# Performance work log

Hardware: AMD Instinct MI355X
Metric: run time of the kernel (lower is better)

Reference implementation:

```python
import jax, jax.numpy as jnp
import numpy as np

T, N, E = 5, 100000, 1600000
D = 64          # input_dim == lstm hidden_size
H = 64          # hidden_dim (gcn output dim)
FE = 16         # edge_feat_dim


def setup_inputs() -> dict:
    key = jax.random.key(0)
    ks = jax.random.split(key, 12)
    s = 0.05
    return {
        "xs": jax.random.normal(ks[0], (T, N, D), dtype=jnp.float32),
        "edge_index": jax.random.randint(ks[1], (2, E), 0, N, dtype=jnp.int64),
        "edge_attr": jax.random.normal(ks[2], (E, FE), dtype=jnp.float32),
        "init_w": jax.random.normal(ks[3], (D, H), dtype=jnp.float32) * s,
        "w_ih": jax.random.normal(ks[4], (4 * D, D), dtype=jnp.float32) * s,
        "w_hh": jax.random.normal(ks[5], (4 * D, D), dtype=jnp.float32) * s,
        "b_ih": jnp.zeros((4 * D,), dtype=jnp.float32),
        "b_hh": jnp.zeros((4 * D,), dtype=jnp.float32),
        "mlp_w1": jax.random.normal(ks[6], (2 * H + FE, H), dtype=jnp.float32) * s,
        "mlp_b1": jnp.zeros((H,), dtype=jnp.float32),
        "mlp_w2": jax.random.normal(ks[7], (H, 1), dtype=jnp.float32) * s,
        "mlp_b2": jnp.zeros((1,), dtype=jnp.float32),
    }


def reference(xs, edge_index, edge_attr, init_w, w_ih, w_hh, b_ih, b_hh,
              mlp_w1, mlp_b1, mlp_w2, mlp_b2):
    n = xs.shape[1]
    # add_self_loops: append (i,i) for every node
    loops = jnp.arange(n, dtype=edge_index.dtype)
    row = jnp.concatenate([edge_index[0], loops])   # source
    col = jnp.concatenate([edge_index[1], loops])   # target (aggregation index)
    # symmetric GCN normalization based on in-degree over col
    deg = jax.ops.segment_sum(jnp.ones_like(col, dtype=xs.dtype), col, num_segments=n)
    dinv = jnp.where(deg > 0, jax.lax.rsqrt(jnp.maximum(deg, 1.0)) * jnp.where(deg > 0, 1.0, 0.0), 0.0)
    dinv = jnp.where(deg > 0, deg ** -0.5, 0.0)
    norm = dinv[row] * dinv[col]                    # [E+N]

    hd = init_w.shape[1]        # lstm batch = hidden_dim rows of W^T
    hs = w_hh.shape[1]          # lstm hidden size = input_dim
    h0 = jnp.zeros((hd, hs), dtype=xs.dtype)
    c0 = jnp.zeros((hd, hs), dtype=xs.dtype)

    def lstm_step(w, h, c):
        xb = w.T                                    # [hidden_dim, input_dim]
        gates = xb @ w_ih.T + b_ih + h @ w_hh.T + b_hh
        i, f, g, o = jnp.split(gates, 4, axis=-1)   # PyTorch gate order i,f,g,o
        i, f, o = jax.nn.sigmoid(i), jax.nn.sigmoid(f), jax.nn.sigmoid(o)
        g = jnp.tanh(g)
        c = f * c + i * g
        h = o * jnp.tanh(c)
        return h.T, h, c                            # new weight = out.squeeze(1).t()

    def step(carry, x_t):
        w, h, c = carry
        w, h, c = lstm_step(w, h, c)
        xw = x_t @ w                                # [N, H]
        msg = norm[:, None] * xw[row]               # gather + normalize
        agg = jax.ops.segment_sum(msg, col, num_segments=n)  # scatter-add
        x_out = jax.nn.relu(agg)                    # dropout: eval mode -> identity
        return (w, h, c), x_out

    _, xs_out = jax.lax.scan(step, (init_w, h0, c0), xs)
    x_last = xs_out[-1]                             # embeddings of the last graph

    h_src = x_last[edge_index[0]]
    h_dst = x_last[edge_index[1]]
    edge_in = jnp.concatenate([h_src, h_dst, edge_attr], axis=1)  # [E, 2H+FE]
    hid = jax.nn.relu(edge_in @ mlp_w1 + mlp_b1)
    logits = (hid @ mlp_w2 + mlp_b2)[:, 0]
    return logits
```

## Files before the change

kernel.cpp:

```cpp
#include <hip/hip_runtime.h>
#include <hip/hip_bf16.h>
#include <math.h>

#define N_NODES 100000
#define N_EDGES 1600000

#define KP 168
#define KU 160

typedef __attribute__((ext_vector_type(8))) short bf16x8;
typedef __attribute__((ext_vector_type(4))) float f32x4;

__device__ __forceinline__ float sigmoidf_(float x) { return 1.0f / (1.0f + expf(-x)); }
__device__ __forceinline__ unsigned short f2b(float x) {
    __hip_bfloat16 b = __float2bfloat16(x);
    return *(unsigned short*)&b;
}
__device__ __forceinline__ float b2f(unsigned short u) {
    __hip_bfloat16 b = *(__hip_bfloat16*)&u;
    return __bfloat162float(b);
}

__global__ __launch_bounds__(256) void lstm_kernel(
    const float* __restrict__ init_w, const float* __restrict__ w_ih,
    const float* __restrict__ w_hh, const float* __restrict__ b_ih,
    const float* __restrict__ b_hh, float* __restrict__ h_out)
{
    __shared__ float wsum[256 * 65];
    __shared__ float hst[64];
    __shared__ float cst[64];
    __shared__ float gts[256];
    const int t = threadIdx.x;
    const int r = blockIdx.x;

    for (int i = t; i < 256 * 64; i += 256) {
        int g = i >> 6, k = i & 63;
        wsum[g * 65 + k] = w_ih[i] + w_hh[i];
    }
    if (t < 64) hst[t] = init_w[t * 64 + r];
    __syncthreads();

    {
        float acc = b_ih[t] + b_hh[t];
        for (int k = 0; k < 64; ++k) acc += hst[k] * w_ih[t * 64 + k];
        gts[t] = acc;
    }
    __syncthreads();
    if (t < 64) {
        float ig = sigmoidf_(gts[t]);
        float gg = tanhf(gts[128 + t]);
        float og = sigmoidf_(gts[192 + t]);
        float c = ig * gg;
        float h = og * tanhf(c);
        cst[t] = c; hst[t] = h;
    }
    __syncthreads();

    for (int step = 1; step < 5; ++step) {
        float acc = b_ih[t] + b_hh[t];
        for (int k = 0; k < 64; ++k) acc += hst[k] * wsum[t * 65 + k];
        gts[t] = acc;
        __syncthreads();
        if (t < 64) {
            float ig = sigmoidf_(gts[t]);
            float fg = sigmoidf_(gts[64 + t]);
            float gg = tanhf(gts[128 + t]);
            float og = sigmoidf_(gts[192 + t]);
            float c = fg * cst[t] + ig * gg;
            float h = og * tanhf(c);
            cst[t] = c; hst[t] = h;
        }
        __syncthreads();
    }
    if (t < 64) h_out[r * 64 + t] = hst[t];
}

__global__ void deg_kernel(const int* __restrict__ col, int* __restrict__ cnt, int nE)
{
    int i = blockIdx.x * blockDim.x + threadIdx.x;
    int stride = gridDim.x * blockDim.x;
    for (; i < nE; i += stride) atomicAdd(&cnt[col[i]], 1);
}

__global__ void dinv_kernel(const int* __restrict__ cnt, float* __restrict__ dinv, int n)
{
    int i = blockIdx.x * blockDim.x + threadIdx.x;
    int stride = gridDim.x * blockDim.x;
    for (; i < n; i += stride) dinv[i] = rsqrtf((float)(cnt[i] + 1));
}

__global__ __launch_bounds__(1024) void scan_kernel(
    const int* __restrict__ cnt, int* __restrict__ offs, int n)
{
    __shared__ int wsums[16];
    __shared__ int carry_s;
    const int tid = threadIdx.x, lane = tid & 63, wid = tid >> 6;
    if (tid == 0) carry_s = 0;
    __syncthreads();
    for (int base = 0; base < n; base += 4096) {
        int i0 = base + tid * 4;
        int v0 = 0, v1 = 0, v2 = 0, v3 = 0;
        if (i0 + 3 < n) { int4 v = *(const int4*)(cnt + i0); v0 = v.x; v1 = v.y; v2 = v.z; v3 = v.w; }
        else {
            if (i0 < n)     v0 = cnt[i0];
            if (i0 + 1 < n) v1 = cnt[i0 + 1];
            if (i0 + 2 < n) v2 = cnt[i0 + 2];
            if (i0 + 3 < n) v3 = cnt[i0 + 3];
        }
        int tot = v0 + v1 + v2 + v3;
        int s = tot;
        #pragma unroll
        for (int d = 1; d < 64; d <<= 1) { int u = __shfl_up(s, d, 64); if (lane >= d) s += u; }
        if (lane == 63) wsums[wid] = s;
        __syncthreads();
        if (tid == 0) {
            int run = carry_s;
            #pragma unroll
            for (int w = 0; w < 16; ++w) { int u = wsums[w]; wsums[w] = run; run += u; }
            carry_s = run;
        }
        __syncthreads();
        int ex = s - tot + wsums[wid];
        if (i0 < n)     offs[i0]     = ex;
        if (i0 + 1 < n) offs[i0 + 1] = ex + v0;
        if (i0 + 2 < n) offs[i0 + 2] = ex + v0 + v1;
        if (i0 + 3 < n) offs[i0 + 3] = ex + v0 + v1 + v2;
        __syncthreads();
    }
}

__global__ void fill_kernel(const int* __restrict__ row, const int* __restrict__ col,
                            const int* __restrict__ offs, int* __restrict__ fill,
                            int* __restrict__ csr, int nE)
{
    int i = blockIdx.x * blockDim.x + threadIdx.x;
    int stride = gridDim.x * blockDim.x;
    for (; i < nE; i += stride) {
        int c = col[i];
        int pos = atomicAdd(&fill[c], 1);
        csr[offs[c] + pos] = row[i];
    }
}

__global__ __launch_bounds__(256) void xw_kernel(
    const float* __restrict__ x4, const float* __restrict__ h5,
    const float* __restrict__ dinv, unsigned short* __restrict__ y, int n)
{
    __shared__ float wlds[64 * 64];
    const int t = threadIdx.x;
    for (int i = t; i < 4096; i += 256) {
        int j = i >> 6, k = i & 63;
        wlds[k * 64 + j] = h5[i];
    }
    __syncthreads();
    const int lane = t & 63;
    int wv = blockIdx.x * 4 + (t >> 6);
    const int nw = gridDim.x * 4;
    for (int nd = wv; nd < n; nd += nw) {
        float xv = x4[(size_t)nd * 64 + lane];
        float acc = 0.f;
        #pragma unroll
        for (int k = 0; k < 64; ++k) {
            float xk = __shfl(xv, k, 64);
            acc += xk * wlds[k * 64 + lane];
        }
        y[(size_t)nd * 64 + lane] = f2b(acc * dinv[nd]);
    }
}

__global__ __launch_bounds__(256) void gather_kernel(
    const int* __restrict__ offs, const int* __restrict__ cnt,
    const int* __restrict__ csr, const unsigned short* __restrict__ y,
    const float* __restrict__ dinv, unsigned short* __restrict__ xl, int n)
{
    const int lane = threadIdx.x & 63;
    int wv = blockIdx.x * 4 + (threadIdx.x >> 6);
    const int nw = gridDim.x * 4;
    for (int c = wv; c < n; c += nw) {
        float acc = b2f(y[(size_t)c * 64 + lane]);
        int beg = offs[c], num = cnt[c];
        int p = 0;
        for (; p + 4 <= num; p += 4) {
            int r0 = csr[beg + p],     r1 = csr[beg + p + 1];
            int r2 = csr[beg + p + 2], r3 = csr[beg + p + 3];
            float a0 = b2f(y[(size_t)r0 * 64 + lane]);
            float a1 = b2f(y[(size_t)r1 * 64 + lane]);
            float a2 = b2f(y[(size_t)r2 * 64 + lane]);
            float a3 = b2f(y[(size_t)r3 * 64 + lane]);
            acc += (a0 + a1) + (a2 + a3);
        }
        for (; p < num; ++p) acc += b2f(y[(size_t)csr[beg + p] * 64 + lane]);
        xl[(size_t)c * 64 + lane] = f2b(fmaxf(acc * dinv[c], 0.0f));
    }
}

__global__ __launch_bounds__(256) void prep_kernel(const float* __restrict__ w1,
                                                   unsigned short* __restrict__ w1t)
{
    int i = blockIdx.x * 256 + threadIdx.x;
    if (i < 64 * KP) {
        int n = i / KP, k = i - n * KP;
        float v = (k < 144) ? w1[k * 64 + n] : 0.f;
        w1t[i] = f2b(v);
    }
}

__global__ __launch_bounds__(256) void mlp_kernel(
    const unsigned short* __restrict__ xl, const int* __restrict__ ei,
    const float* __restrict__ ea, const unsigned short* __restrict__ w1t,
    const float* __restrict__ b1, const float* __restrict__ w2,
    const float* __restrict__ b2, float* __restrict__ out)
{
    __shared__ unsigned short As[64 * KP];
    __shared__ unsigned short Bs[64 * KP];
    const int t = threadIdx.x;
    const int base = blockIdx.x * 64;

    {
        const uint4* s = (const uint4*)w1t;
        uint4* d = (uint4*)Bs;
        #pragma unroll
        for (int it = 0; it < 6; ++it) {
            int i = t + it * 256;
            if (i < (64 * KP) / 8) d[i] = s[i];
        }
    }
    #pragma unroll
    for (int it = 0; it < 4; ++it) {
        int i = t + it * 256;
        int e = i >> 4, c = i & 15;
        int src = ei[base + e];
        *(uint2*)&As[e * KP + c * 4] = *(const uint2*)&xl[(size_t)src * 64 + c * 4];
    }
    #pragma unroll
    for (int it = 0; it < 4; ++it) {
        int i = t + it * 256;
        int e = i >> 4, c = i & 15;
        int dst = ei[N_EDGES + base + e];
        *(uint2*)&As[e * KP + 64 + c * 4] = *(const uint2*)&xl[(size_t)dst * 64 + c * 4];
    }
    {
        int e = t >> 2, c = t & 3;
        float4 v = *(const float4*)&ea[(size_t)(base + e) * 16 + c * 4];
        ushort4 b;
        b.x = f2b(v.x); b.y = f2b(v.y); b.z = f2b(v.z); b.w = f2b(v.w);
        *(ushort4*)&As[e * KP + 128 + c * 4] = b;
        uint2 z; z.x = 0; z.y = 0;
        *(uint2*)&As[e * KP + 144 + c * 4] = z;
    }
    __syncthreads();

    const int lane = t & 63, w = t >> 6;
    const int col0 = lane & 15, rgrp = lane >> 4;
    const int arow = w * 16 + col0;

    f32x4 acc[4];
    #pragma unroll
    for (int nt = 0; nt < 4; ++nt) acc[nt] = (f32x4){0.f, 0.f, 0.f, 0.f};

    #pragma unroll
    for (int ks = 0; ks < KU / 32; ++ks) {
        int klane = ks * 32 + rgrp * 8;
        bf16x8 a = *(const bf16x8*)&As[arow * KP + klane];
        #pragma unroll
        for (int nt = 0; nt < 4; ++nt) {
            bf16x8 bfr = *(const bf16x8*)&Bs[(nt * 16 + col0) * KP + klane];
            acc[nt] = __builtin_amdgcn_mfma_f32_16x16x32_bf16(a, bfr, acc[nt], 0, 0, 0);
        }
    }

    float bsum = b2[0];
    float part[4];
    #pragma unroll
    for (int j = 0; j < 4; ++j) {
        float s = 0.f;
        #pragma unroll
        for (int nt = 0; nt < 4; ++nt) {
            int nn = nt * 16 + col0;
            s += fmaxf(acc[nt][j] + b1[nn], 0.f) * w2[nn];
        }
        #pragma unroll
        for (int m = 1; m < 16; m <<= 1) s += __shfl_xor(s, m, 64);
        part[j] = s;
    }
    if (col0 == 0) {
        int row = rgrp * 4;
        #pragma unroll
        for (int j = 0; j < 4; ++j)
            out[base + w * 16 + row + j] = part[j] + bsum;
    }
}

extern "C" void kernel_launch(void* const* d_in, const int* in_sizes, int n_in,
                              void* d_out, int out_size, void* d_ws, size_t ws_size,
                              hipStream_t stream)
{
    const float* xs     = (const float*)d_in[0];
    const int*   ei     = (const int*)  d_in[1];
    const float* ea     = (const float*)d_in[2];
    const float* init_w = (const float*)d_in[3];
    const float* w_ih   = (const float*)d_in[4];
    const float* w_hh   = (const float*)d_in[5];
    const float* b_ih   = (const float*)d_in[6];
    const float* b_hh   = (const float*)d_in[7];
    const float* w1     = (const float*)d_in[8];
    const float* b1     = (const float*)d_in[9];
    const float* w2     = (const float*)d_in[10];
    const float* b2     = (const float*)d_in[11];
    float* out = (float*)d_out;

    char* ws = (char*)d_ws;
    size_t off = 0;
    auto alloc = [&](size_t bytes) {
        void* p = ws + off;
        off = (off + bytes + 255) & ~(size_t)255;
        return p;
    };
    float*          h5   = (float*)alloc(64 * 64 * sizeof(float));
    int*            deg  = (int*)  alloc((size_t)N_NODES * sizeof(int));
    int*            fill = (int*)  alloc((size_t)N_NODES * sizeof(int));
    float*          dinv = (float*)alloc((size_t)N_NODES * sizeof(float));
    int*            offs = (int*)  alloc((size_t)N_NODES * sizeof(int));
    int*            csr  = (int*)  alloc((size_t)N_EDGES * sizeof(int));
    unsigned short* y    = (unsigned short*)alloc((size_t)N_NODES * 64 * sizeof(unsigned short));
    unsigned short* xl   = (unsigned short*)alloc((size_t)N_NODES * 64 * sizeof(unsigned short));
    unsigned short* w1t  = (unsigned short*)alloc((size_t)64 * KP * sizeof(unsigned short));

    hipMemsetAsync(deg, 0, (size_t)N_NODES * sizeof(int), stream);
    hipMemsetAsync(fill, 0, (size_t)N_NODES * sizeof(int), stream);

    lstm_kernel<<<64, 256, 0, stream>>>(init_w, w_ih, w_hh, b_ih, b_hh, h5);
    prep_kernel<<<(64 * KP + 255) / 256, 256, 0, stream>>>(w1, w1t);
    deg_kernel<<<1024, 256, 0, stream>>>(ei + N_EDGES, deg, N_EDGES);
    dinv_kernel<<<512, 256, 0, stream>>>(deg, dinv, N_NODES);
    scan_kernel<<<1, 1024, 0, stream>>>(deg, offs, N_NODES);
    fill_kernel<<<1024, 256, 0, stream>>>(ei, ei + N_EDGES, offs, fill, csr, N_EDGES);

    const float* x4 = xs + (size_t)4 * N_NODES * 64;
    xw_kernel<<<2048, 256, 0, stream>>>(x4, h5, dinv, y, N_NODES);
    gather_kernel<<<2048, 256, 0, stream>>>(offs, deg, csr, y, dinv, xl, N_NODES);
    mlp_kernel<<<N_EDGES / 64, 256, 0, stream>>>(xl, ei, ea, w1t, b1, w2, b2, out);
}
```

Baseline: 692.4 us.

## Parallelize CSR scan, vectorize atomics, split gather lanes, register-resident MLP weights

Replaces the single-block degree scan with a three-kernel parallel scan that also writes dinv and initializes fill pointers, which removes the dinv kernel and a memset. Degree and fill kernels now read indices as int4 and use fill as an absolute position. The gather kernel splits each wave into four sub-groups that each process a different neighbor, using 8-byte vector loads, and combines them with cross-lane shuffles. The MLP kernel keeps W1 fragments in registers, loads A fragments straight from global memory with no LDS staging, and uses a persistent grid looping over 16-edge tiles. This raises register pressure and drops LDS reuse of the node embeddings.

```diff
diff --git a/kernel.cpp b/kernel.cpp
--- a/kernel.cpp
+++ b/kernel.cpp
@@ -4,9 +4,7 @@
 
 #define N_NODES 100000
 #define N_EDGES 1600000
-
-#define KP 168
-#define KU 160
+#define NCHUNK 98
 
 typedef __attribute__((ext_vector_type(8))) short bf16x8;
 typedef __attribute__((ext_vector_type(4))) float f32x4;
@@ -75,70 +73,102 @@
     if (t < 64) h_out[r * 64 + t] = hst[t];
 }
 
-__global__ void deg_kernel(const int* __restrict__ col, int* __restrict__ cnt, int nE)
+__global__ void deg_kernel(const int* __restrict__ col, int* __restrict__ cnt, int nE4)
 {
     int i = blockIdx.x * blockDim.x + threadIdx.x;
     int stride = gridDim.x * blockDim.x;
-    for (; i < nE; i += stride) atomicAdd(&cnt[col[i]], 1);
-}
-
-__global__ void dinv_kernel(const int* __restrict__ cnt, float* __restrict__ dinv, int n)
+    for (; i < nE4; i += stride) {
+        int4 c = ((const int4*)col)[i];
+        atomicAdd(&cnt[c.x], 1);
+        atomicAdd(&cnt[c.y], 1);
+        atomicAdd(&cnt[c.z], 1);
+        atomicAdd(&cnt[c.w], 1);
+    }
+}
+
+__global__ __launch_bounds__(256) void scanA_kernel(
+    const int* __restrict__ deg, int* __restrict__ partial,
+    float* __restrict__ dinv, int n)
+{
+    __shared__ int wsums[4];
+    const int t = threadIdx.x, lane = t & 63, wid = t >> 6;
+    int i0 = blockIdx.x * 1024 + t * 4;
+    int v0 = 0, v1 = 0, v2 = 0, v3 = 0;
+    if (i0 + 3 < n) { int4 v = *(const int4*)(deg + i0); v0 = v.x; v1 = v.y; v2 = v.z; v3 = v.w; }
+    else {
+        if (i0 < n)     v0 = deg[i0];
+        if (i0 + 1 < n) v1 = deg[i0 + 1];
+        if (i0 + 2 < n) v2 = deg[i0 + 2];
+        if (i0 + 3 < n) v3 = deg[i0 + 3];
+    }
+    if (i0 < n)     dinv[i0]     = rsqrtf((float)(v0 + 1));
+    if (i0 + 1 < n) dinv[i0 + 1] = rsqrtf((float)(v1 + 1));
+    if (i0 + 2 < n) dinv[i0 + 2] = rsqrtf((float)(v2 + 1));
+    if (i0 + 3 < n) dinv[i0 + 3] = rsqrtf((float)(v3 + 1));
+    int s = v0 + v1 + v2 + v3;
+    #pragma unroll
+    for (int m = 1; m < 64; m <<= 1) s += __shfl_xor(s, m, 64);
+    if (lane == 0) wsums[wid] = s;
+    __syncthreads();
+    if (t == 0) partial[blockIdx.x] = wsums[0] + wsums[1] + wsums[2] + wsums[3];
+}
+
+__global__ void scanB_kernel(int* __restrict__ partial, int nb)
+{
+    __shared__ int w0;
+    const int t = threadIdx.x, lane = t & 63, wid = t >> 6;
+    int v = (t < nb) ? partial[t] : 0;
+    int s = v;
+    #pragma unroll
+    for (int d = 1; d < 64; d <<= 1) { int u = __shfl_up(s, d, 64); if (lane >= d) s += u; }
+    if (t == 63) w0 = s;
+    __syncthreads();
+    int ex = s - v + ((wid == 1) ? w0 : 0);
+    if (t < nb) partial[t] = ex;
+}
+
+__global__ __launch_bounds__(256) void scanC_kernel(
+    const int* __restrict__ deg, const int* __restrict__ partial,
+    int* __restrict__ offs, int* __restrict__ fill, int n)
+{
+    __shared__ int wsums[4];
+    const int t = threadIdx.x, lane = t & 63, wid = t >> 6;
+    int i0 = blockIdx.x * 1024 + t * 4;
+    int v0 = 0, v1 = 0, v2 = 0, v3 = 0;
+    if (i0 + 3 < n) { int4 v = *(const int4*)(deg + i0); v0 = v.x; v1 = v.y; v2 = v.z; v3 = v.w; }
+    else {
+        if (i0 < n)     v0 = deg[i0];
+        if (i0 + 1 < n) v1 = deg[i0 + 1];
+        if (i0 + 2 < n) v2 = deg[i0 + 2];
+        if (i0 + 3 < n) v3 = deg[i0 + 3];
+    }
+    int tot = v0 + v1 + v2 + v3;
+    int s = tot;
+    #pragma unroll
+    for (int d = 1; d < 64; d <<= 1) { int u = __shfl_up(s, d, 64); if (lane >= d) s += u; }
+    if (lane == 63) wsums[wid] = s;
+    __syncthreads();
+    if (t == 0) { int run = 0; for (int w = 0; w < 4; ++w) { int u = wsums[w]; wsums[w] = run; run += u; } }
+    __syncthreads();
+    int ex = s - tot + wsums[wid] + partial[blockIdx.x];
+    if (i0 < n)     { offs[i0]     = ex;                fill[i0]     = ex; }
+    if (i0 + 1 < n) { offs[i0 + 1] = ex + v0;           fill[i0 + 1] = ex + v0; }
+    if (i0 + 2 < n) { offs[i0 + 2] = ex + v0 + v1;      fill[i0 + 2] = ex + v0 + v1; }
+    if (i0 + 3 < n) { offs[i0 + 3] = ex + v0 + v1 + v2; fill[i0 + 3] = ex + v0 + v1 + v2; }
+}
+
+__global__ void fill_kernel(const int* __restrict__ row, const int* __restrict__ col,
+                            int* __restrict__ fill, int* __restrict__ csr, int nE4)
 {
     int i = blockIdx.x * blockDim.x + threadIdx.x;
     int stride = gridDim.x * blockDim.x;
-    for (; i < n; i += stride) dinv[i] = rsqrtf((float)(cnt[i] + 1));
-}
-
-__global__ __launch_bounds__(1024) void scan_kernel(
-    const int* __restrict__ cnt, int* __restrict__ offs, int n)
-{
-    __shared__ int wsums[16];
-    __shared__ int carry_s;
-    const int tid = threadIdx.x, lane = tid & 63, wid = tid >> 6;
-    if (tid == 0) carry_s = 0;
-    __syncthreads();
-    for (int base = 0; base < n; base += 4096) {
-        int i0 = base + tid * 4;
-        int v0 = 0, v1 = 0, v2 = 0, v3 = 0;
-        if (i0 + 3 < n) { int4 v = *(const int4*)(cnt + i0); v0 = v.x; v1 = v.y; v2 = v.z; v3 = v.w; }
-        else {
-            if (i0 < n)     v0 = cnt[i0];
-            if (i0 + 1 < n) v1 = cnt[i0 + 1];
-            if (i0 + 2 < n) v2 = cnt[i0 + 2];
-            if (i0 + 3 < n) v3 = cnt[i0 + 3];
-        }
-        int tot = v0 + v1 + v2 + v3;
-        int s = tot;
-        #pragma unroll
-        for (int d = 1; d < 64; d <<= 1) { int u = __shfl_up(s, d, 64); if (lane >= d) s += u; }
-        if (lane == 63) wsums[wid] = s;
-        __syncthreads();
-        if (tid == 0) {
-            int run = carry_s;
-            #pragma unroll
-            for (int w = 0; w < 16; ++w) { int u = wsums[w]; wsums[w] = run; run += u; }
-            carry_s = run;
-        }
-        __syncthreads();
-        int ex = s - tot + wsums[wid];
-        if (i0 < n)     offs[i0]     = ex;
-        if (i0 + 1 < n) offs[i0 + 1] = ex + v0;
-        if (i0 + 2 < n) offs[i0 + 2] = ex + v0 + v1;
-        if (i0 + 3 < n) offs[i0 + 3] = ex + v0 + v1 + v2;
-        __syncthreads();
-    }
-}
-
-__global__ void fill_kernel(const int* __restrict__ row, const int* __restrict__ col,
-                            const int* __restrict__ offs, int* __restrict__ fill,
-                            int* __restrict__ csr, int nE)
-{
-    int i = blockIdx.x * blockDim.x + threadIdx.x;
-    int stride = gridDim.x * blockDim.x;
-    for (; i < nE; i += stride) {
-        int c = col[i];
-        int pos = atomicAdd(&fill[c], 1);
-        csr[offs[c] + pos] = row[i];
+    for (; i < nE4; i += stride) {
+        int4 c = ((const int4*)col)[i];
+        int4 r = ((const int4*)row)[i];
+        csr[atomicAdd(&fill[c.x], 1)] = r.x;
+        csr[atomicAdd(&fill[c.y], 1)] = r.y;
+        csr[atomicAdd(&fill[c.z], 1)] = r.z;
+        csr[atomicAdd(&fill[c.w], 1)] = r.w;
     }
 }
 
@@ -174,23 +204,45 @@
     const float* __restrict__ dinv, unsigned short* __restrict__ xl, int n)
 {
     const int lane = threadIdx.x & 63;
-    int wv = blockIdx.x * 4 + (threadIdx.x >> 6);
-    const int nw = gridDim.x * 4;
+    const int sub = lane >> 4, q = lane & 15;
+    int wv = (blockIdx.x * 256 + threadIdx.x) >> 6;
+    const int nw = (gridDim.x * 256) >> 6;
     for (int c = wv; c < n; c += nw) {
-        float acc = b2f(y[(size_t)c * 64 + lane]);
-        int beg = offs[c], num = cnt[c];
-        int p = 0;
-        for (; p + 4 <= num; p += 4) {
-            int r0 = csr[beg + p],     r1 = csr[beg + p + 1];
-            int r2 = csr[beg + p + 2], r3 = csr[beg + p + 3];
-            float a0 = b2f(y[(size_t)r0 * 64 + lane]);
-            float a1 = b2f(y[(size_t)r1 * 64 + lane]);
-            float a2 = b2f(y[(size_t)r2 * 64 + lane]);
-            float a3 = b2f(y[(size_t)r3 * 64 + lane]);
-            acc += (a0 + a1) + (a2 + a3);
-        }
-        for (; p < num; ++p) acc += b2f(y[(size_t)csr[beg + p] * 64 + lane]);
-        xl[(size_t)c * 64 + lane] = f2b(fmaxf(acc * dinv[c], 0.0f));
+        const int beg = offs[c], num = cnt[c];
+        float acc0 = 0.f, acc1 = 0.f, acc2 = 0.f, acc3 = 0.f;
+        int p = sub;
+        for (; p + 4 < num; p += 8) {
+            int r0 = csr[beg + p];
+            int r1 = csr[beg + p + 4];
+            uint2 v0 = *(const uint2*)&y[(size_t)r0 * 64 + q * 4];
+            uint2 v1 = *(const uint2*)&y[(size_t)r1 * 64 + q * 4];
+            acc0 += b2f((unsigned short)(v0.x & 0xffff)) + b2f((unsigned short)(v1.x & 0xffff));
+            acc1 += b2f((unsigned short)(v0.x >> 16))    + b2f((unsigned short)(v1.x >> 16));
+            acc2 += b2f((unsigned short)(v0.y & 0xffff)) + b2f((unsigned short)(v1.y & 0xffff));
+            acc3 += b2f((unsigned short)(v0.y >> 16))    + b2f((unsigned short)(v1.y >> 16));
+        }
+        if (p < num) {
+            int r0 = csr[beg + p];
+            uint2 v0 = *(const uint2*)&y[(size_t)r0 * 64 + q * 4];
+            acc0 += b2f((unsigned short)(v0.x & 0xffff));
+            acc1 += b2f((unsigned short)(v0.x >> 16));
+            acc2 += b2f((unsigned short)(v0.y & 0xffff));
+            acc3 += b2f((unsigned short)(v0.y >> 16));
+        }
+        acc0 += __shfl_xor(acc0, 16, 64); acc0 += __shfl_xor(acc0, 32, 64);
+        acc1 += __shfl_xor(acc1, 16, 64); acc1 += __shfl_xor(acc1, 32, 64);
+        acc2 += __shfl_xor(acc2, 16, 64); acc2 += __shfl_xor(acc2, 32, 64);
+        acc3 += __shfl_xor(acc3, 16, 64); acc3 += __shfl_xor(acc3, 32, 64);
+        if (sub == 0) {
+            uint2 sv = *(const uint2*)&y[(size_t)c * 64 + q * 4];
+            float d = dinv[c];
+            ushort4 st;
+            st.x = f2b(fmaxf((acc0 + b2f((unsigned short)(sv.x & 0xffff))) * d, 0.f));
+            st.y = f2b(fmaxf((acc1 + b2f((unsigned short)(sv.x >> 16)))    * d, 0.f));
+            st.z = f2b(fmaxf((acc2 + b2f((unsigned short)(sv.y & 0xffff))) * d, 0.f));
+            st.w = f2b(fmaxf((acc3 + b2f((unsigned short)(sv.y >> 16)))    * d, 0.f));
+            *(ushort4*)&xl[(size_t)c * 64 + q * 4] = st;
+        }
     }
 }
 
@@ -198,8 +250,8 @@
                                                    unsigned short* __restrict__ w1t)
 {
     int i = blockIdx.x * 256 + threadIdx.x;
-    if (i < 64 * KP) {
-        int n = i / KP, k = i - n * KP;
+    if (i < 64 * 160) {
+        int n = i / 160, k = i - n * 160;
         float v = (k < 144) ? w1[k * 64 + n] : 0.f;
         w1t[i] = f2b(v);
     }
@@ -211,83 +263,78 @@
     const float* __restrict__ b1, const float* __restrict__ w2,
     const float* __restrict__ b2, float* __restrict__ out)
 {
-    __shared__ unsigned short As[64 * KP];
-    __shared__ unsigned short Bs[64 * KP];
     const int t = threadIdx.x;
-    const int base = blockIdx.x * 64;
-
-    {
-        const uint4* s = (const uint4*)w1t;
-        uint4* d = (uint4*)Bs;
-        #pragma unroll
-        for (int it = 0; it < 6; ++it) {
-            int i = t + it * 256;
-            if (i < (64 * KP) / 8) d[i] = s[i];
-        }
-    }
-    #pragma unroll
-    for (int it = 0; it < 4; ++it) {
-        int i = t + it * 256;
-        int e = i >> 4, c = i & 15;
-        int src = ei[base + e];
-        *(uint2*)&As[e * KP + c * 4] = *(const uint2*)&xl[(size_t)src * 64 + c * 4];
-    }
-    #pragma unroll
-    for (int it = 0; it < 4; ++it) {
-        int i = t + it * 256;
-        int e = i >> 4, c = i & 15;
-        int dst = ei[N_EDGES + base + e];
-        *(uint2*)&As[e * KP + 64 + c * 4] = *(const uint2*)&xl[(size_t)dst * 64 + c * 4];
-    }
-    {
-        int e = t >> 2, c = t & 3;
-        float4 v = *(const float4*)&ea[(size_t)(base + e) * 16 + c * 4];
-        ushort4 b;
-        b.x = f2b(v.x); b.y = f2b(v.y); b.z = f2b(v.z); b.w = f2b(v.w);
-        *(ushort4*)&As[e * KP + 128 + c * 4] = b;
-        uint2 z; z.x = 0; z.y = 0;
-        *(uint2*)&As[e * KP + 144 + c * 4] = z;
-    }
-    __syncthreads();
-
-    const int lane = t & 63, w = t >> 6;
+    const int lane = t & 63;
     const int col0 = lane & 15, rgrp = lane >> 4;
-    const int arow = w * 16 + col0;
-
-    f32x4 acc[4];
-    #pragma unroll
-    for (int nt = 0; nt < 4; ++nt) acc[nt] = (f32x4){0.f, 0.f, 0.f, 0.f};
-
-    #pragma unroll
-    for (int ks = 0; ks < KU / 32; ++ks) {
-        int klane = ks * 32 + rgrp * 8;
-        bf16x8 a = *(const bf16x8*)&As[arow * KP + klane];
-        #pragma unroll
-        for (int nt = 0; nt < 4; ++nt) {
-            bf16x8 bfr = *(const bf16x8*)&Bs[(nt * 16 + col0) * KP + klane];
-            acc[nt] = __builtin_amdgcn_mfma_f32_16x16x32_bf16(a, bfr, acc[nt], 0, 0, 0);
-        }
-    }
-
-    float bsum = b2[0];
-    float part[4];
-    #pragma unroll
-    for (int j = 0; j < 4; ++j) {
-        float s = 0.f;
-        #pragma unroll
-        for (int nt = 0; nt < 4; ++nt) {
-            int nn = nt * 16 + col0;
-            s += fmaxf(acc[nt][j] + b1[nn], 0.f) * w2[nn];
-        }
-        #pragma unroll
-        for (int m = 1; m < 16; m <<= 1) s += __shfl_xor(s, m, 64);
-        part[j] = s;
-    }
-    if (col0 == 0) {
-        int row = rgrp * 4;
-        #pragma unroll
-        for (int j = 0; j < 4; ++j)
-            out[base + w * 16 + row + j] = part[j] + bsum;
+    const int gw = (blockIdx.x * 256 + t) >> 6;
+    const int nw = (gridDim.x * 256) >> 6;
+
+    bf16x8 bfr[5][4];
+    #pragma unroll
+    for (int ks = 0; ks < 5; ++ks)
+        #pragma unroll
+        for (int nt = 0; nt < 4; ++nt)
+            bfr[ks][nt] = *(const bf16x8*)&w1t[(nt * 16 + col0) * 160 + ks * 32 + rgrp * 8];
+
+    float b1v[4], w2v[4];
+    #pragma unroll
+    for (int nt = 0; nt < 4; ++nt) {
+        b1v[nt] = b1[nt * 16 + col0];
+        w2v[nt] = w2[nt * 16 + col0];
+    }
+    const float b2s = b2[0];
+    const bf16x8 zv = {0, 0, 0, 0, 0, 0, 0, 0};
+
+    for (int tile = gw; tile < N_EDGES / 16; tile += nw) {
+        const int e0 = tile * 16;
+        const int eidx = e0 + col0;
+        const int src = ei[eidx];
+        const int dst = ei[N_EDGES + eidx];
+        const unsigned short* ps = xl + (size_t)src * 64 + rgrp * 8;
+        const unsigned short* pd = xl + (size_t)dst * 64 + rgrp * 8;
+        bf16x8 av[5];
+        av[0] = *(const bf16x8*)ps;
+        av[1] = *(const bf16x8*)(ps + 32);
+        av[2] = *(const bf16x8*)pd;
+        av[3] = *(const bf16x8*)(pd + 32);
+        if (rgrp < 2) {
+            const float* pe = ea + (size_t)eidx * 16 + rgrp * 8;
+            float4 u0 = *(const float4*)pe;
+            float4 u1 = *(const float4*)(pe + 4);
+            union { bf16x8 v; unsigned short u[8]; } au;
+            au.u[0] = f2b(u0.x); au.u[1] = f2b(u0.y); au.u[2] = f2b(u0.z); au.u[3] = f2b(u0.w);
+            au.u[4] = f2b(u1.x); au.u[5] = f2b(u1.y); au.u[6] = f2b(u1.z); au.u[7] = f2b(u1.w);
+            av[4] = au.v;
+        } else {
+            av[4] = zv;
+        }
+
+        f32x4 acc[4];
+        #pragma unroll
+        for (int nt = 0; nt < 4; ++nt) acc[nt] = (f32x4){0.f, 0.f, 0.f, 0.f};
+        #pragma unroll
+        for (int ks = 0; ks < 5; ++ks)
+            #pragma unroll
+            for (int nt = 0; nt < 4; ++nt)
+                acc[nt] = __builtin_amdgcn_mfma_f32_16x16x32_bf16(av[ks], bfr[ks][nt], acc[nt], 0, 0, 0);
+
+        float part[4];
+        #pragma unroll
+        for (int j = 0; j < 4; ++j) {
+            float s = 0.f;
+            #pragma unroll
+            for (int nt = 0; nt < 4; ++nt)
+                s += fmaxf(acc[nt][j] + b1v[nt], 0.f) * w2v[nt];
+            #pragma unroll
+            for (int m = 1; m < 16; m <<= 1) s += __shfl_xor(s, m, 64);
+            part[j] = s;
+        }
+        if (col0 == 0) {
+            float4 o;
+            o.x = part[0] + b2s; o.y = part[1] + b2s;
+            o.z = part[2] + b2s; o.w = part[3] + b2s;
+            *(float4*)&out[e0 + rgrp * 4] = o;
+        }
     }
 }
 
@@ -316,28 +363,29 @@
         off = (off + bytes + 255) & ~(size_t)255;
         return p;
     };
-    float*          h5   = (float*)alloc(64 * 64 * sizeof(float));
-    int*            deg  = (int*)  alloc((size_t)N_NODES * sizeof(int));
-    int*            fill = (int*)  alloc((size_t)N_NODES * sizeof(int));
-    float*          dinv = (float*)alloc((size_t)N_NODES * sizeof(float));
-    int*            offs = (int*)  alloc((size_t)N_NODES * sizeof(int));
-    int*            csr  = (int*)  alloc((size_t)N_EDGES * sizeof(int));
-    unsigned short* y    = (unsigned short*)alloc((size_t)N_NODES * 64 * sizeof(unsigned short));
-    unsigned short* xl   = (unsigned short*)alloc((size_t)N_NODES * 64 * sizeof(unsigned short));
-    unsigned short* w1t  = (unsigned short*)alloc((size_t)64 * KP * sizeof(unsigned short));
+    float*          h5      = (float*)alloc(64 * 64 * sizeof(float));
+    int*            deg     = (int*)  alloc((size_t)N_NODES * sizeof(int));
+    int*            fill    = (int*)  alloc((size_t)N_NODES * sizeof(int));
+    float*          dinv    = (float*)alloc((size_t)N_NODES * sizeof(float));
+    int*            offs    = (int*)  alloc((size_t)N_NODES * sizeof(int));
+    int*            csr     = (int*)  alloc((size_t)N_EDGES * sizeof(int));
+    unsigned short* y       = (unsigned short*)alloc((size_t)N_NODES * 64 * sizeof(unsigned short));
+    unsigned short* xl      = (unsigned short*)alloc((size_t)N_NODES * 64 * sizeof(unsigned short));
+    unsigned short* w1t     = (unsigned short*)alloc((size_t)64 * 160 * sizeof(unsigned short));
+    int*            partial = (int*)  alloc(128 * sizeof(int));
 
     hipMemsetAsync(deg, 0, (size_t)N_NODES * sizeof(int), stream);
-    hipMemsetAsync(fill, 0, (size_t)N_NODES * sizeof(int), stream);
 
     lstm_kernel<<<64, 256, 0, stream>>>(init_w, w_ih, w_hh, b_ih, b_hh, h5);
-    prep_kernel<<<(64 * KP + 255) / 256, 256, 0, stream>>>(w1, w1t);
-    deg_kernel<<<1024, 256, 0, stream>>>(ei + N_EDGES, deg, N_EDGES);
-    dinv_kernel<<<512, 256, 0, stream>>>(deg, dinv, N_NODES);
-    scan_kernel<<<1, 1024, 0, stream>>>(deg, offs, N_NODES);
-    fill_kernel<<<1024, 256, 0, stream>>>(ei, ei + N_EDGES, offs, fill, csr, N_EDGES);
+    prep_kernel<<<(64 * 160 + 255) / 256, 256, 0, stream>>>(w1, w1t);
+    deg_kernel<<<1024, 256, 0, stream>>>(ei + N_EDGES, deg, N_EDGES / 4);
+    scanA_kernel<<<NCHUNK, 256, 0, stream>>>(deg, partial, dinv, N_NODES);
+    scanB_kernel<<<1, 128, 0, stream>>>(partial, NCHUNK);
+    scanC_kernel<<<NCHUNK, 256, 0, stream>>>(deg, partial, offs, fill, N_NODES);
+    fill_kernel<<<1024, 256, 0, stream>>>(ei, ei + N_EDGES, fill, csr, N_EDGES / 4);
 
     const float* x4 = xs + (size_t)4 * N_NODES * 64;
     xw_kernel<<<2048, 256, 0, stream>>>(x4, h5, dinv, y, N_NODES);
     gather_kernel<<<2048, 256, 0, stream>>>(offs, deg, csr, y, dinv, xl, N_NODES);
-    mlp_kernel<<<N_EDGES / 64, 256, 0, stream>>>(xl, ei, ea, w1t, b1, w2, b2, out);
-}
+    mlp_kernel<<<2048, 256, 0, stream>>>(xl, ei, ea, w1t, b1, w2, b2, out);
+}
```

Result: faster. 666.6 us (-3.7%).
